# Kernel tuning notes

Hardware: AMD Instinct MI355X
Metric: run time of the kernel (lower is better)

Reference implementation:

```python
import jax, jax.numpy as jnp
import numpy as np

D_MODEL = 2048
N_HEAD = 16
HEAD_DIM = D_MODEL // N_HEAD
D_FF = 8192
SEQ = 2048
PAST = 2048
BATCH = 2
LN_EPS = 1e-5


def setup_inputs() -> dict:
    key = jax.random.key(0)
    ks = jax.random.split(key, 16)
    s = 0.02  # weight init scale
    return {
        "x": jax.random.normal(ks[0], (SEQ, BATCH, D_MODEL), jnp.float32),
        "k_cache": jax.random.normal(ks[1], (PAST, BATCH, N_HEAD, HEAD_DIM), jnp.float32),
        "v_cache": jax.random.normal(ks[2], (PAST, BATCH, N_HEAD, HEAD_DIM), jnp.float32),
        "mask": jnp.zeros((SEQ, PAST + SEQ), jnp.float32),
        "q_w": jax.random.normal(ks[3], (D_MODEL, D_MODEL), jnp.float32) * s,
        "q_b": jnp.zeros((D_MODEL,), jnp.float32),
        "k_w": jax.random.normal(ks[4], (D_MODEL, D_MODEL), jnp.float32) * s,
        "k_b": jnp.zeros((D_MODEL,), jnp.float32),
        "v_w": jax.random.normal(ks[5], (D_MODEL, D_MODEL), jnp.float32) * s,
        "v_b": jnp.zeros((D_MODEL,), jnp.float32),
        "o_w": jax.random.normal(ks[6], (D_MODEL, D_MODEL), jnp.float32) * s,
        "o_b": jnp.zeros((D_MODEL,), jnp.float32),
        "ln1_g": jnp.ones((D_MODEL,), jnp.float32),
        "ln1_b": jnp.zeros((D_MODEL,), jnp.float32),
        "ln2_g": jnp.ones((D_MODEL,), jnp.float32),
        "ln2_b": jnp.zeros((D_MODEL,), jnp.float32),
        "w1": jax.random.normal(ks[7], (D_MODEL, D_FF), jnp.float32) * s,
        "b1": jnp.zeros((D_FF,), jnp.float32),
        "w2": jax.random.normal(ks[8], (D_FF, D_MODEL), jnp.float32) * s,
        "b2": jnp.zeros((D_MODEL,), jnp.float32),
    }


def _layernorm(y, g, b):
    m = jnp.mean(y, axis=-1, keepdims=True)
    v = jnp.var(y, axis=-1, keepdims=True)  # biased var, matches torch LayerNorm
    return (y - m) * jax.lax.rsqrt(v + LN_EPS) * g + b


def reference(x, k_cache, v_cache, mask, q_w, q_b, k_w, k_b, v_w, v_b, o_w, o_b,
              ln1_g, ln1_b, ln2_g, ln2_b, w1, b1, w2, b2):
    S, B, D = x.shape
    H, hd = N_HEAD, HEAD_DIM

    x_norm = _layernorm(x, ln1_g, ln1_b)
    q = (x_norm @ q_w + q_b).reshape(S, B, H, hd)
    k = (x_norm @ k_w + k_b).reshape(S, B, H, hd)
    v = (x_norm @ v_w + v_b).reshape(S, B, H, hd)

    k_full = jnp.concatenate([k_cache, k], axis=0)  # [T,B,H,hd], T = past+S
    v_full = jnp.concatenate([v_cache, v], axis=0)

    # scores: [B,H,S,T]
    scores = jnp.einsum('sbhd,tbhd->bhst', q, k_full) / (hd ** 0.5)
    scores = scores + mask  # mask [S,T] broadcasts over B,H
    attn = jax.nn.softmax(scores, axis=-1)
    out = jnp.einsum('bhst,tbhd->sbhd', attn, v_full).reshape(S, B, D)
    x = x + out @ o_w + o_b

    h = _layernorm(x, ln2_g, ln2_b)
    x = x + jax.nn.gelu(h @ w1 + b1, approximate=False) @ w2 + b2
    return (x, k_full, v_full)
```

## Files before the change

kernel.cpp:

```cpp
#include <hip/hip_runtime.h>
#include <hip/hip_bf16.h>


typedef __bf16 bf16x8 __attribute__((ext_vector_type(8)));
typedef float f32x4 __attribute__((ext_vector_type(4)));
typedef float f32x16 __attribute__((ext_vector_type(16)));
typedef unsigned int u32;

__device__ __forceinline__ unsigned short f2bf(float f) {
  union { float f; unsigned u; } v; v.f = f;
  return (unsigned short)((v.u + 0x7FFFu + ((v.u >> 16) & 1u)) >> 16);
}

__device__ __forceinline__ float fexp2(float x) {
#if __has_builtin(__builtin_amdgcn_exp2f)
  return __builtin_amdgcn_exp2f(x);
#else
  float r;
  asm volatile("v_exp_f32 %0, %1\ns_nop 0" : "=v"(r) : "v"(x));
  return r;
#endif
}

__device__ __forceinline__ float fast_gelu(float x) {
  const float u = 0.7978845608028654f * fmaf(0.044715f * x * x, x, x);
  const float e = fexp2(fminf(u * 2.885390081777927f, 126.f));
  float rcp;
  asm("v_rcp_f32 %0, %1" : "=v"(rcp) : "v"(e + 1.f));
  return x * e * rcp;
}

__device__ __forceinline__ void gl16(const void* g, void* l) {
  __builtin_amdgcn_global_load_lds((__attribute__((address_space(1))) void*)g,
                                   (__attribute__((address_space(3))) void*)l,
                                   16, 0, 0);
}

__global__ __launch_bounds__(256) void wconvT(const float* __restrict__ W,
                                              unsigned short* __restrict__ Wt,
                                              int K, int N) {
  __shared__ float tl[32][33];
  const int k0 = blockIdx.x * 32, n0 = blockIdx.y * 32;
  const int x = threadIdx.x & 31, y = threadIdx.x >> 5;
  for (int i = 0; i < 4; ++i)
    tl[y + i * 8][x] = W[(size_t)(k0 + y + i * 8) * N + n0 + x];
  __syncthreads();
  for (int i = 0; i < 4; ++i)
    Wt[(size_t)(n0 + y + i * 8) * K + k0 + x] = f2bf(tl[x][y + i * 8]);
}

__global__ __launch_bounds__(256) void prep_k(
    const float* __restrict__ x, const float* __restrict__ ln1g,
    const float* __restrict__ ln1b, unsigned short* __restrict__ xn,
    const float* __restrict__ kc, unsigned short* __restrict__ kf,
    float* __restrict__ out_k,
    const float* __restrict__ vc, unsigned short* __restrict__ vft,
    float* __restrict__ out_v,
    const float* __restrict__ mask, u32* __restrict__ mflags,
    const float* __restrict__ q_w, const float* __restrict__ k_w,
    const float* __restrict__ v_w, const float* __restrict__ o_w,
    unsigned short* __restrict__ Wt) {
  __shared__ float tl[32][33];
  __shared__ float red[8];
  const int blk = blockIdx.x;
  const int tid = threadIdx.x;

  if (blk < 4096) {
    const int row = blk;
    const float4* xr = (const float4*)(x + (size_t)row * 2048);
    const float4 xa = xr[tid], xb = xr[tid + 256];
    float s = xa.x + xa.y + xa.z + xa.w + xb.x + xb.y + xb.z + xb.w;
    float q = xa.x * xa.x + xa.y * xa.y + xa.z * xa.z + xa.w * xa.w +
              xb.x * xb.x + xb.y * xb.y + xb.z * xb.z + xb.w * xb.w;
    for (int off = 32; off; off >>= 1) {
      s += __shfl_xor(s, off);
      q += __shfl_xor(q, off);
    }
    const int wv = tid >> 6, ln = tid & 63;
    if (ln == 0) { red[wv] = s; red[4 + wv] = q; }
    __syncthreads();
    s = red[0] + red[1] + red[2] + red[3];
    q = red[4] + red[5] + red[6] + red[7];
    const float mean = s * (1.f / 2048.f);
    const float rstd = rsqrtf(q * (1.f / 2048.f) - mean * mean + 1e-5f);
    const float4 g0 = ((const float4*)ln1g)[tid], g1 = ((const float4*)ln1g)[tid + 256];
    const float4 b0 = ((const float4*)ln1b)[tid], b1 = ((const float4*)ln1b)[tid + 256];
    ushort4 o0, o1;
    o0.x = f2bf((xa.x - mean) * rstd * g0.x + b0.x);
    o0.y = f2bf((xa.y - mean) * rstd * g0.y + b0.y);
    o0.z = f2bf((xa.z - mean) * rstd * g0.z + b0.z);
    o0.w = f2bf((xa.w - mean) * rstd * g0.w + b0.w);
    o1.x = f2bf((xb.x - mean) * rstd * g1.x + b1.x);
    o1.y = f2bf((xb.y - mean) * rstd * g1.y + b1.y);
    o1.z = f2bf((xb.z - mean) * rstd * g1.z + b1.z);
    o1.w = f2bf((xb.w - mean) * rstd * g1.w + b1.w);
    ((ushort4*)(xn + (size_t)row * 2048))[tid] = o0;
    ((ushort4*)(xn + (size_t)row * 2048))[tid + 256] = o1;
  } else if (blk < 12288) {
    const size_t e = ((size_t)(blk - 4096) * 256 + tid) * 4;
    const int r = (int)(e >> 11), c = (int)(e & 2047);
    const int t = r >> 1, b = r & 1, h = c >> 7, d = c & 127;
    const float4 v = *(const float4*)(kc + e);
    ushort4 o;
    o.x = f2bf(v.x); o.y = f2bf(v.y); o.z = f2bf(v.z); o.w = f2bf(v.w);
    *(ushort4*)(kf + ((size_t)((b * 16 + h) * 4096 + t)) * 128 + d) = o;
    *(float4*)(out_k + (size_t)r * 2048 + c) = v;
  } else if (blk < 20480) {
    const int i = blk - 12288;
    const int t0 = (i & 63) * 32, d0 = ((i >> 6) & 3) * 32, bh = i >> 8;
    const int b = bh >> 4, h = bh & 15;
    const int xx = tid & 31, yy = tid >> 5;
    for (int ii = 0; ii < 4; ++ii) {
      const int t = t0 + yy + ii * 8, d = d0 + xx;
      const float v = vc[((size_t)(t * 2 + b) * 16 + h) * 128 + d];
      tl[yy + ii * 8][xx] = v;
      out_v[((size_t)(t * 2 + b) * 16 + h) * 128 + d] = v;
    }
    __syncthreads();
    for (int ii = 0; ii < 4; ++ii) {
      const int d = d0 + yy + ii * 8, t = t0 + xx;
      vft[((size_t)bh * 128 + d) * 4096 + t] = f2bf(tl[xx][yy + ii * 8]);
    }
  } else if (blk < 20736) {
    const int mb = blk - 20480;
    const float4* p = (const float4*)mask + (size_t)mb * 8192 + tid;
    int nz = 0;
#pragma unroll
    for (int ii = 0; ii < 32; ++ii) {
      const float4 v = p[ii * 256];
      nz |= (v.x != 0.f) | (v.y != 0.f) | (v.z != 0.f) | (v.w != 0.f);
    }
    const int r = __syncthreads_or(nz);
    if (tid == 0) mflags[mb] = (u32)r;
  } else {
    const int i = blk - 20736;
    const int k0 = (i & 63) * 32, n0 = ((i >> 6) & 63) * 32, z = i >> 12;
    const float* W = z == 0 ? q_w : (z == 1 ? k_w : (z == 2 ? v_w : o_w));
    unsigned short* dst = Wt + (size_t)z * 2048 * 2048;
    const int xx = tid & 31, yy = tid >> 5;
    for (int ii = 0; ii < 4; ++ii)
      tl[yy + ii * 8][xx] = W[(size_t)(k0 + yy + ii * 8) * 2048 + n0 + xx];
    __syncthreads();
    for (int ii = 0; ii < 4; ++ii)
      dst[(size_t)(n0 + yy + ii * 8) * 2048 + k0 + xx] = f2bf(tl[xx][yy + ii * 8]);
  }
}

__global__ __launch_bounds__(256) void prep2_k(
    const float* __restrict__ x1, const float* __restrict__ ln2g,
    const float* __restrict__ ln2b, unsigned short* __restrict__ hn,
    const float* __restrict__ w1, unsigned short* __restrict__ w1t,
    const float* __restrict__ w2, unsigned short* __restrict__ w2t) {
  __shared__ float tl[32][33];
  __shared__ float red[8];
  const int blk = blockIdx.x;
  const int tid = threadIdx.x;

  if (blk < 4096) {
    const int row = blk;
    const float4* xr = (const float4*)(x1 + (size_t)row * 2048);
    const float4 xa = xr[tid], xb = xr[tid + 256];
    float s = xa.x + xa.y + xa.z + xa.w + xb.x + xb.y + xb.z + xb.w;
    float q = xa.x * xa.x + xa.y * xa.y + xa.z * xa.z + xa.w * xa.w +
              xb.x * xb.x + xb.y * xb.y + xb.z * xb.z + xb.w * xb.w;
    for (int off = 32; off; off >>= 1) {
      s += __shfl_xor(s, off);
      q += __shfl_xor(q, off);
    }
    const int wv = tid >> 6, ln = tid & 63;
    if (ln == 0) { red[wv] = s; red[4 + wv] = q; }
    __syncthreads();
    s = red[0] + red[1] + red[2] + red[3];
    q = red[4] + red[5] + red[6] + red[7];
    const float mean = s * (1.f / 2048.f);
    const float rstd = rsqrtf(q * (1.f / 2048.f) - mean * mean + 1e-5f);
    const float4 g0 = ((const float4*)ln2g)[tid], g1 = ((const float4*)ln2g)[tid + 256];
    const float4 b0 = ((const float4*)ln2b)[tid], b1 = ((const float4*)ln2b)[tid + 256];
    ushort4 o0, o1;
    o0.x = f2bf((xa.x - mean) * rstd * g0.x + b0.x);
    o0.y = f2bf((xa.y - mean) * rstd * g0.y + b0.y);
    o0.z = f2bf((xa.z - mean) * rstd * g0.z + b0.z);
    o0.w = f2bf((xa.w - mean) * rstd * g0.w + b0.w);
    o1.x = f2bf((xb.x - mean) * rstd * g1.x + b1.x);
    o1.y = f2bf((xb.y - mean) * rstd * g1.y + b1.y);
    o1.z = f2bf((xb.z - mean) * rstd * g1.z + b1.z);
    o1.w = f2bf((xb.w - mean) * rstd * g1.w + b1.w);
    ((ushort4*)(hn + (size_t)row * 2048))[tid] = o0;
    ((ushort4*)(hn + (size_t)row * 2048))[tid + 256] = o1;
  } else if (blk < 20480) {
    const int i = blk - 4096;
    const int k0 = (i & 63) * 32, n0 = (i >> 6) * 32;
    const int xx = tid & 31, yy = tid >> 5;
    for (int ii = 0; ii < 4; ++ii)
      tl[yy + ii * 8][xx] = w1[(size_t)(k0 + yy + ii * 8) * 8192 + n0 + xx];
    __syncthreads();
    for (int ii = 0; ii < 4; ++ii)
      w1t[(size_t)(n0 + yy + ii * 8) * 2048 + k0 + xx] = f2bf(tl[xx][yy + ii * 8]);
  } else {
    const int i = blk - 20480;
    const int k0 = (i & 255) * 32, n0 = (i >> 8) * 32;
    const int xx = tid & 31, yy = tid >> 5;
    for (int ii = 0; ii < 4; ++ii)
      tl[yy + ii * 8][xx] = w2[(size_t)(k0 + yy + ii * 8) * 2048 + n0 + xx];
    __syncthreads();
    for (int ii = 0; ii < 4; ++ii)
      w2t[(size_t)(n0 + yy + ii * 8) * 8192 + k0 + xx] = f2bf(tl[xx][yy + ii * 8]);
  }
}

template <int TAG, int EPI>
__global__ __launch_bounds__(512, 2) void gemm8p(
    const unsigned short* __restrict__ A, const unsigned short* __restrict__ Bt,
    const float* __restrict__ bias, const float* __restrict__ bias2,
    const float* __restrict__ bias3,
    float* __restrict__ Cf, unsigned short* __restrict__ Cb,
    float* __restrict__ of2, unsigned short* __restrict__ pb2,
    unsigned short* __restrict__ pb3, int N, int K) {
  __shared__ unsigned short sA[2][256 * 64];
  __shared__ unsigned short sB[2][256 * 64];
  const int tid = threadIdx.x;
  const int wv = tid >> 6, ln = tid & 63;
  const int wm = wv >> 2, wn = wv & 3;
  const int nwg = gridDim.x;
  const int bid = blockIdx.x;
  const int wk = (bid & 7) * (nwg >> 3) + (bid >> 3);
  const int nmt = 16;
  const int m0 = (wk & (nmt - 1)) * 256, n0 = (wk / nmt) * 256;
  const int NT = K >> 6, NI = NT >> 1;

  f32x4 acc[8][4] = {};
  bf16x8 af[4][2], bfr[2][2];

  auto ST = [&](int t, int which, int bb) {
    if (t >= NT) return;
    const unsigned short* G = (which < 2) ? A : Bt;
    const int base0 = ((which < 2) ? m0 : n0) + (which & 1) * 128;
    char* dst = (char*)((which < 2) ? &sA[bb][0] : &sB[bb][0]) + (which & 1) * 16384;
    const size_t kb = (size_t)t * 64;
#pragma unroll
    for (int c = 0; c < 2; ++c) {
      const int o = tid * 16 + c * 8192;
      const int row = o >> 7;
      const int cb = (o & 127) ^ ((row & 7) << 4);
      gl16((const char*)G + ((size_t)(base0 + row) * K + kb) * 2 + cb, dst + o);
    }
  };
  auto LDA = [&](int bb, int mh) {
    const char* base = (const char*)&sA[bb][0];
#pragma unroll
    for (int i = 0; i < 4; ++i) {
      const int r = wm * 128 + mh * 64 + i * 16 + (ln & 15);
#pragma unroll
      for (int kk = 0; kk < 2; ++kk) {
        int aa = (r << 7) + ((ln >> 4) << 4) + kk * 64;
        aa ^= (r & 7) << 4;
        af[i][kk] = *(const bf16x8*)(base + aa);
      }
    }
  };
  auto LDB = [&](int bb, int nh) {
    const char* base = (const char*)&sB[bb][0];
#pragma unroll
    for (int j = 0; j < 2; ++j) {
      const int r = wn * 64 + nh * 32 + j * 16 + (ln & 15);
#pragma unroll
      for (int kk = 0; kk < 2; ++kk) {
        int aa = (r << 7) + ((ln >> 4) << 4) + kk * 64;
        aa ^= (r & 7) << 4;
        bfr[j][kk] = *(const bf16x8*)(base + aa);
      }
    }
  };
  auto MM = [&](int mh, int nh) {
    __builtin_amdgcn_s_setprio(1);
#pragma unroll
    for (int i = 0; i < 4; ++i)
#pragma unroll
      for (int j = 0; j < 2; ++j)
#pragma unroll
        for (int kk = 0; kk < 2; ++kk)
          acc[mh * 4 + i][nh * 2 + j] = __builtin_amdgcn_mfma_f32_16x16x32_bf16(
              af[i][kk], bfr[j][kk], acc[mh * 4 + i][nh * 2 + j], 0, 0, 0);
    __builtin_amdgcn_s_setprio(0);
  };
#define BAR() __builtin_amdgcn_s_barrier()
#define VM2() asm volatile("s_waitcnt vmcnt(2)" ::: "memory")
#define VM0() asm volatile("s_waitcnt vmcnt(0)" ::: "memory")

  ST(0, 0, 0); ST(0, 1, 0); ST(0, 2, 0); ST(0, 3, 0); ST(1, 0, 1);
  VM2();
  BAR();

#pragma unroll 1
  for (int it = 0; it < NI; ++it) {
    const int t1 = 2 * it + 1, t2 = 2 * it + 2, t3 = 2 * it + 3;
    const bool lastit = (it == NI - 1);
    LDA(0, 0); LDB(0, 0); ST(t1, 1, 1); BAR(); MM(0, 0); BAR();
    LDB(0, 1);            ST(t1, 2, 1); BAR(); MM(0, 1); BAR();
    LDA(0, 1);            ST(t1, 3, 1); BAR(); MM(1, 1); BAR();
    LDB(0, 0);            ST(t2, 0, 0); BAR(); MM(1, 0);
    if (lastit) VM0(); else VM2();
    BAR();
    LDA(1, 0); LDB(1, 0); ST(t2, 1, 0); BAR(); MM(0, 0); BAR();
    LDB(1, 1);            ST(t2, 2, 0); BAR(); MM(0, 1); BAR();
    LDA(1, 1);            ST(t2, 3, 0); BAR(); MM(1, 1); BAR();
    LDB(1, 0);            ST(t3, 0, 1); BAR(); MM(1, 0);
    if (!lastit) VM2();
    BAR();
  }
#undef BAR
#undef VM2
#undef VM0

  const int lr = (ln >> 4) << 2, lc = ln & 15;
  if (EPI == 0) {
    const int seg = n0 >> 11;
    const float* bp = seg == 0 ? bias : (seg == 1 ? bias2 : bias3);
#pragma unroll
    for (int f = 0; f < 8; ++f) {
#pragma unroll
      for (int j = 0; j < 4; ++j) {
        const int nn = (n0 & 2047) + wn * 64 + j * 16 + lc;
        const int h = nn >> 7, d = nn & 127;
        const float bv = bp[nn];
#pragma unroll
        for (int r = 0; r < 4; ++r) {
          const int m = m0 + wm * 128 + f * 16 + lr + r;
          const int s = m >> 1, b = m & 1;
          const float v = acc[f][j][r] + bv;
          if (seg == 0) {
            Cb[((size_t)(b * 16 + h) * 2048 + s) * 128 + d] = f2bf(v);
          } else if (seg == 1) {
            pb2[((size_t)(b * 16 + h) * 4096 + 2048 + s) * 128 + d] = f2bf(v);
            Cf[((size_t)((2048 + s) * 2 + b) * 16 + h) * 128 + d] = v;
          } else {
            pb3[((size_t)(b * 16 + h) * 128 + d) * 4096 + 2048 + s] = f2bf(v);
            of2[((size_t)((2048 + s) * 2 + b) * 16 + h) * 128 + d] = v;
          }
        }
      }
    }
  } else {
    char* wbase = (wv < 4) ? (char*)&sA[0][0] + wv * 16384
                           : (char*)&sB[0][0] + (wv - 4) * 16384;
#pragma unroll
    for (int f = 0; f < 8; ++f) {
#pragma unroll
      for (int j = 0; j < 4; ++j) {
        const int nl = j * 16 + lc;
        const float bv = bias[n0 + wn * 64 + nl];
#pragma unroll
        for (int r = 0; r < 4; ++r) {
          const int ml = f * 16 + lr + r;
          const float v = fast_gelu(acc[f][j][r] + bv);
          *(unsigned short*)(wbase + ml * 128 + ((nl * 2) ^ ((ml & 7) << 4))) =
              f2bf(v);
        }
      }
    }
    __syncthreads();
#pragma unroll
    for (int p = 0; p < 16; ++p) {
      const int row = p * 16 + (tid >> 5);
      const int nn = (tid & 31) * 8;
      const int wvv = (row >> 7) * 4 + (nn >> 6);
      const char* rb = (wvv < 4) ? (const char*)&sA[0][0] + wvv * 16384
                                 : (const char*)&sB[0][0] + (wvv - 4) * 16384;
      const int ml = row & 127, nl = nn & 63;
      const int4 val = *(const int4*)(rb + ml * 128 + ((nl * 2) ^ ((ml & 7) << 4)));
      *(int4*)((char*)Cb + ((size_t)(m0 + row) * N + n0 + nn) * 2) = val;
    }
  }
}

template <int TAG, int EPI>
__global__ __launch_bounds__(512, 2) void gemm8n(
    const unsigned short* __restrict__ A, const unsigned short* __restrict__ Bt,
    const float* __restrict__ bias, const float* __restrict__ Rsd,
    float* __restrict__ Cf, int N, int K) {
  __shared__ unsigned short sA[2][128 * 64];
  __shared__ unsigned short sB[2][256 * 64];
  const int tid = threadIdx.x;
  const int wv = tid >> 6, ln = tid & 63;
  const int wm = wv >> 2, wn = wv & 3;
  const int nwg = gridDim.x;
  const int bid = blockIdx.x;
  const int wk = (bid & 7) * (nwg >> 3) + (bid >> 3);
  const int m0 = (wk & 31) * 128, n0 = (wk >> 5) * 256;
  const int NT = K >> 6;

  f32x4 acc[4][4] = {};
  bf16x8 af[2][2], bfr[2][2];

  auto ST = [&](int t, int which, int bb) {
    if (t >= NT) return;
    const unsigned short* G = (which == 0) ? A : Bt;
    const int base0 = (which == 0) ? m0 : (which == 1 ? n0 : n0 + 128);
    char* dst = (which == 0) ? (char*)&sA[bb][0]
                             : (char*)&sB[bb][0] + (which - 1) * 16384;
    const size_t kb = (size_t)t * 64;
#pragma unroll
    for (int c = 0; c < 2; ++c) {
      const int o = tid * 16 + c * 8192;
      const int row = o >> 7;
      const int cb = (o & 127) ^ ((row & 7) << 4);
      gl16((const char*)G + ((size_t)(base0 + row) * K + kb) * 2 + cb, dst + o);
    }
  };
  auto LDA = [&](int bb, int mh) {
    const char* base = (const char*)&sA[bb][0];
#pragma unroll
    for (int i = 0; i < 2; ++i) {
      const int r = wm * 64 + mh * 32 + i * 16 + (ln & 15);
#pragma unroll
      for (int kk = 0; kk < 2; ++kk) {
        int aa = (r << 7) + ((ln >> 4) << 4) + kk * 64;
        aa ^= (r & 7) << 4;
        af[i][kk] = *(const bf16x8*)(base + aa);
      }
    }
  };
  auto LDB = [&](int bb, int nh) {
    const char* base = (const char*)&sB[bb][0];
#pragma unroll
    for (int j = 0; j < 2; ++j) {
      const int r = wn * 64 + nh * 32 + j * 16 + (ln & 15);
#pragma unroll
      for (int kk = 0; kk < 2; ++kk) {
        int aa = (r << 7) + ((ln >> 4) << 4) + kk * 64;
        aa ^= (r & 7) << 4;
        bfr[j][kk] = *(const bf16x8*)(base + aa);
      }
    }
  };
  auto MM = [&](int mh, int nh) {
    __builtin_amdgcn_s_setprio(1);
#pragma unroll
    for (int i = 0; i < 2; ++i)
#pragma unroll
      for (int j = 0; j < 2; ++j)
#pragma unroll
        for (int kk = 0; kk < 2; ++kk)
          acc[mh * 2 + i][nh * 2 + j] = __builtin_amdgcn_mfma_f32_16x16x32_bf16(
              af[i][kk], bfr[j][kk], acc[mh * 2 + i][nh * 2 + j], 0, 0, 0);
    __builtin_amdgcn_s_setprio(0);
  };
#define BAR() __builtin_amdgcn_s_barrier()
#define VM2() asm volatile("s_waitcnt vmcnt(2)" ::: "memory")
#define VM0() asm volatile("s_waitcnt vmcnt(0)" ::: "memory")

  ST(0, 0, 0); ST(0, 1, 0); ST(0, 2, 0); ST(1, 0, 1);
  VM2();
  BAR();

#pragma unroll 1
  for (int t = 0; t < NT; ++t) {
    const int cur = t & 1;
    LDA(cur, 0); LDB(cur, 0); ST(t + 1, 1, cur ^ 1); BAR(); MM(0, 0); BAR();
    LDB(cur, 1); ST(t + 1, 2, cur ^ 1); BAR(); MM(0, 1); BAR();
    LDA(cur, 1); BAR(); MM(1, 1); BAR();
    LDB(cur, 0); ST(t + 2, 0, cur); BAR(); MM(1, 0);
    if (t >= NT - 2) VM0(); else VM2();
    BAR();
  }
#undef BAR
#undef VM2
#undef VM0

  const int lr = (ln >> 4) << 2, lc = ln & 15;
#pragma unroll
  for (int i = 0; i < 4; ++i) {
#pragma unroll
    for (int j = 0; j < 4; ++j) {
      const int n = n0 + wn * 64 + j * 16 + lc;
      const float bv = bias[n];
#pragma unroll
      for (int r = 0; r < 4; ++r) {
        const int m = m0 + wm * 64 + i * 16 + lr + r;
        const float v = acc[i][j][r] + bv + Rsd[(size_t)m * N + n];
        Cf[(size_t)m * N + n] = v;
      }
    }
  }
}

__global__ __launch_bounds__(256, 2) void attn6(
    const unsigned short* __restrict__ Q,
    const unsigned short* __restrict__ Kf,
    const unsigned short* __restrict__ Vt,
    const float* __restrict__ mask,
    const u32* __restrict__ flags,
    unsigned short* __restrict__ ctx) {
  __shared__ __attribute__((aligned(16))) char smem[65536];
  const int tid = threadIdx.x;
  const int wv = tid >> 6;
  const int ln = tid & 63;
  const int q = ln & 31;
  const int hi = ln >> 5;
  const int sw = (q & 7) << 4;
  const int bh = blockIdx.y;
  const int s0w = blockIdx.x * 128 + wv * 32;

  const int mnz = __syncthreads_or((int)flags[tid]);

  bf16x8 qreg[8];
  {
    const char* qsrc = (const char*)Q +
        ((size_t)bh * 2048 + s0w + q) * 256 + (hi << 4);
#pragma unroll
    for (int kk = 0; kk < 8; ++kk) qreg[kk] = *(const bf16x8*)(qsrc + kk * 32);
  }

  const char* kp[8];
  const char* vp[4];
#pragma unroll
  for (int kk = 0; kk < 8; ++kk)
    kp[kk] = smem + (q << 8) + (((kk << 5) + (hi << 4)) ^ sw);
#pragma unroll
  for (int kk = 0; kk < 4; ++kk)
    vp[kk] = smem + 32768 + (q << 7) + (((kk << 5) + (hi << 4)) ^ sw);

  const char* Kg;
  const char* Vg;
  {
    const int oo = tid * 16;
    const int kr = oo >> 8, kc = oo & 255;
    Kg = (const char*)Kf + (size_t)bh * 4096 * 256 + (size_t)kr * 256 +
         (kc ^ ((kr & 7) << 4));
    const int vr = oo >> 7, vc = oo & 127;
    Vg = (const char*)Vt + (size_t)bh * 128 * 8192 + (size_t)vr * 8192 +
         (vc ^ ((vr & 7) << 4));
  }
  char* kdst = smem + tid * 16;
  char* vdst = smem + 32768 + tid * 16;

#define STG(BUF)                                               \
  do {                                                         \
    _Pragma("unroll") for (int is = 0; is < 4; ++is) {         \
      gl16(Kg + is * 4096, kdst + (BUF) + is * 4096);          \
      gl16(Vg + (size_t)is * 262144, vdst + (BUF) + is * 4096);\
    }                                                          \
    Kg += 16384; Vg += 128;                                    \
  } while (0)
#define BARR() __builtin_amdgcn_s_barrier()
#define VMW8() asm volatile("s_waitcnt vmcnt(8)" ::: "memory")
#define VMW0() asm volatile("s_waitcnt vmcnt(0)" ::: "memory")

  f32x16 acc[4] = {};
  float m = -1e30f, l = 0.f;
  const float KLOG = 0.127517445f;

  auto tile = [&](int BUF, int it) {
    f32x16 sc0, sc1;
    {
      f32x16 za = {}, zb = {}, zc = {}, zd = {};
      __builtin_amdgcn_s_setprio(1);
#pragma unroll
      for (int kk = 0; kk < 4; ++kk) {
        za = __builtin_amdgcn_mfma_f32_32x32x16_bf16(
            *(const bf16x8*)(kp[kk] + BUF), qreg[kk], za, 0, 0, 0);
        zb = __builtin_amdgcn_mfma_f32_32x32x16_bf16(
            *(const bf16x8*)(kp[kk + 4] + BUF), qreg[kk + 4], zb, 0, 0, 0);
        zc = __builtin_amdgcn_mfma_f32_32x32x16_bf16(
            *(const bf16x8*)(kp[kk] + BUF + 8192), qreg[kk], zc, 0, 0, 0);
        zd = __builtin_amdgcn_mfma_f32_32x32x16_bf16(
            *(const bf16x8*)(kp[kk + 4] + BUF + 8192), qreg[kk + 4], zd, 0, 0, 0);
      }
      __builtin_amdgcn_s_setprio(0);
      sc0 = za + zb;
      sc1 = zc + zd;
    }

    if (mnz) {
      const float rs = 11.313708498984761f;
#pragma unroll
      for (int r = 0; r < 16; ++r) {
        const int tt = it * 64 + ((r & 3) + ((r >> 2) << 3) + (hi << 2));
        sc0[r] = fmaf(mask[(size_t)(s0w + q) * 4096 + tt], rs, sc0[r]);
        sc1[r] = fmaf(mask[(size_t)(s0w + q) * 4096 + tt + 32], rs, sc1[r]);
      }
    }

    float pmax = sc0[0];
#pragma unroll
    for (int r = 1; r < 16; ++r) pmax = fmaxf(pmax, sc0[r]);
#pragma unroll
    for (int r = 0; r < 16; ++r) pmax = fmaxf(pmax, sc1[r]);
    pmax = fmaxf(pmax, __shfl_xor(pmax, 32));
    if (__any(pmax > m + 90.5f)) {
      const float mn = fmaxf(m, pmax);
      const float corr = fexp2((m - mn) * KLOG);
      m = mn; l *= corr;
#pragma unroll
      for (int d4 = 0; d4 < 4; ++d4)
#pragma unroll
        for (int e = 0; e < 16; ++e) acc[d4][e] *= corr;
    }
    const float mk = m * KLOG;
    float rsum = 0.f;
#pragma unroll
    for (int r = 0; r < 16; ++r) {
      const float e = fexp2(fmaf(sc0[r], KLOG, -mk));
      sc0[r] = e;
      rsum += e;
    }
#pragma unroll
    for (int r = 0; r < 16; ++r) {
      const float e = fexp2(fmaf(sc1[r], KLOG, -mk));
      sc1[r] = e;
      rsum += e;
    }
    rsum += __shfl_xor(rsum, 32);
    l += rsum;

    bf16x8 pw[4];
#pragma unroll
    for (int kk = 0; kk < 4; ++kk) {
      const int rb = (kk & 1) * 8;
      u32 w0, w1, w2, w3;
      if (kk < 2) {
        asm("v_cvt_pk_bf16_f32 %0, %1, %2" : "=v"(w0) : "v"(sc0[rb + 0]), "v"(sc0[rb + 1]));
        asm("v_cvt_pk_bf16_f32 %0, %1, %2" : "=v"(w1) : "v"(sc0[rb + 2]), "v"(sc0[rb + 3]));
        asm("v_cvt_pk_bf16_f32 %0, %1, %2" : "=v"(w2) : "v"(sc0[rb + 4]), "v"(sc0[rb + 5]));
        asm("v_cvt_pk_bf16_f32 %0, %1, %2" : "=v"(w3) : "v"(sc0[rb + 6]), "v"(sc0[rb + 7]));
      } else {
        asm("v_cvt_pk_bf16_f32 %0, %1, %2" : "=v"(w0) : "v"(sc1[rb + 0]), "v"(sc1[rb + 1]));
        asm("v_cvt_pk_bf16_f32 %0, %1, %2" : "=v"(w1) : "v"(sc1[rb + 2]), "v"(sc1[rb + 3]));
        asm("v_cvt_pk_bf16_f32 %0, %1, %2" : "=v"(w2) : "v"(sc1[rb + 4]), "v"(sc1[rb + 5]));
        asm("v_cvt_pk_bf16_f32 %0, %1, %2" : "=v"(w3) : "v"(sc1[rb + 6]), "v"(sc1[rb + 7]));
      }
      asm("v_permlane32_swap_b32 %0, %1" : "+v"(w0), "+v"(w2));
      asm("v_permlane32_swap_b32 %0, %1" : "+v"(w1), "+v"(w3));
      union { u32 u[4]; bf16x8 b; } pk;
      pk.u[0] = w0; pk.u[1] = w1; pk.u[2] = w2; pk.u[3] = w3;
      pw[kk] = pk.b;
    }

#pragma unroll
    for (int d4 = 0; d4 < 4; ++d4) {
      __builtin_amdgcn_s_setprio(1);
#pragma unroll
      for (int kk = 0; kk < 4; ++kk)
        acc[d4] = __builtin_amdgcn_mfma_f32_32x32x16_bf16(
            *(const bf16x8*)(vp[kk] + BUF + d4 * 4096), pw[kk], acc[d4], 0, 0, 0);
      __builtin_amdgcn_s_setprio(0);
    }
  };

  STG(0);
  STG(16384);
#pragma unroll 1
  for (int it2 = 0; it2 < 31; ++it2) {
    VMW8(); BARR();
    tile(0, 2 * it2);
    BARR();
    STG(0);
    VMW8(); BARR();
    tile(16384, 2 * it2 + 1);
    BARR();
    STG(16384);
  }
  VMW8(); BARR();
  tile(0, 62);
  BARR();
  VMW0(); BARR();
  tile(16384, 63);
#undef STG
#undef BARR
#undef VMW8
#undef VMW0

  const float inv = 1.f / l;
  const int b = bh >> 4, h = bh & 15;
  unsigned short* crow = ctx + ((size_t)(s0w + q) * 2 + b) * 2048 + h * 128;
#pragma unroll
  for (int d4 = 0; d4 < 4; ++d4)
#pragma unroll
    for (int rq = 0; rq < 4; ++rq) {
      ushort4 o;
      o.x = f2bf(acc[d4][rq * 4 + 0] * inv);
      o.y = f2bf(acc[d4][rq * 4 + 1] * inv);
      o.z = f2bf(acc[d4][rq * 4 + 2] * inv);
      o.w = f2bf(acc[d4][rq * 4 + 3] * inv);
      *(ushort4*)(crow + d4 * 32 + rq * 8 + hi * 4) = o;
    }
}

extern "C" void kernel_launch(void* const* d_in, const int* in_sizes, int n_in,
                              void* d_out, int out_size, void* d_ws, size_t ws_size,
                              hipStream_t stream) {
  const float* x    = (const float*)d_in[0];
  const float* kc   = (const float*)d_in[1];
  const float* vc   = (const float*)d_in[2];
  const float* mask = (const float*)d_in[3];
  const float* q_w  = (const float*)d_in[4];
  const float* q_b  = (const float*)d_in[5];
  const float* k_w  = (const float*)d_in[6];
  const float* k_b  = (const float*)d_in[7];
  const float* v_w  = (const float*)d_in[8];
  const float* v_b  = (const float*)d_in[9];
  const float* o_w  = (const float*)d_in[10];
  const float* o_b  = (const float*)d_in[11];
  const float* ln1g = (const float*)d_in[12];
  const float* ln1b = (const float*)d_in[13];
  const float* ln2g = (const float*)d_in[14];
  const float* ln2b = (const float*)d_in[15];
  const float* w1   = (const float*)d_in[16];
  const float* b1   = (const float*)d_in[17];
  const float* w2   = (const float*)d_in[18];
  const float* b2   = (const float*)d_in[19];

  float* out_x = (float*)d_out;
  float* out_k = out_x + (size_t)8388608;
  float* out_v = out_k + (size_t)16777216;

  char* ws = (char*)d_ws;
  unsigned short* kf  = (unsigned short*)(ws);
  unsigned short* vft = (unsigned short*)(ws + 33554432);
  unsigned short* Wt  = (unsigned short*)(ws + 67108864);
  float*          x1  = (float*)(ws + 100663296);
  unsigned short* mid = (unsigned short*)ws;
  u32* mflags = (u32*)(ws + 100663296);

  unsigned short* xn  = (unsigned short*)d_out;
  unsigned short* ctx = xn;
  unsigned short* qb  = (unsigned short*)((char*)d_out + 16777216);
  unsigned short* hn  = qb;

  const bool bigws = ws_size >= (size_t)167772160;
  unsigned short* w2t = bigws ? (unsigned short*)(ws + 134217728) : Wt;

  const dim3 b256(256);

  prep_k<<<37120, b256, 0, stream>>>(x, ln1g, ln1b, xn, kc, kf, out_k,
                                     vc, vft, out_v, mask, mflags,
                                     q_w, k_w, v_w, o_w, Wt);

  gemm8p<0, 0><<<384, dim3(512), 0, stream>>>(
      xn, Wt, q_b, k_b, v_b, out_k, qb, out_v, kf, vft, 6144, 2048);

  attn6<<<dim3(16, 32), b256, 0, stream>>>(qb, kf, vft, mask, mflags, ctx);

  gemm8n<1, 1><<<256, dim3(512), 0, stream>>>(
      ctx, Wt + (size_t)6144 * 2048, o_b, x, x1, 2048, 2048);

  prep2_k<<<bigws ? 36864 : 20480, b256, 0, stream>>>(
      x1, ln2g, ln2b, hn, w1, Wt, w2, w2t);

  gemm8p<2, 2><<<512, dim3(512), 0, stream>>>(
      hn, Wt, b1, nullptr, nullptr, nullptr, mid, nullptr, nullptr, nullptr,
      8192, 2048);

  if (!bigws) wconvT<<<dim3(256, 64), b256, 0, stream>>>(w2, Wt, 8192, 2048);

  gemm8n<3, 1><<<256, dim3(512), 0, stream>>>(
      mid, w2t, b2, x1, out_x, 2048, 8192);
}
```

Before: 842.7 us.

## Split attention over KV length into two halves with a combine kernel

The attention kernel now splits the 4096-key sequence into two halves along a new grid z dimension, so twice as many blocks run. Each block uses half the shared memory with separate K and V staging phases, and launch bounds ask for higher occupancy. Each half writes unnormalized bf16 partial outputs plus its running max and sum, and a new combine kernel merges them into the context buffer. This is meant to fix under-filled compute units from the 512-block grid, at the cost of an extra launch, extra memory traffic, bf16 rounding of the partials, and less prefetch depth.

Measured after the change: 1.240 ms. 47.1% more time.

```diff
diff --git a/kernel.cpp b/kernel.cpp
--- a/kernel.cpp
+++ b/kernel.cpp
@@ -10,6 +10,11 @@
 __device__ __forceinline__ unsigned short f2bf(float f) {
   union { float f; unsigned u; } v; v.f = f;
   return (unsigned short)((v.u + 0x7FFFu + ((v.u >> 16) & 1u)) >> 16);
+}
+
+__device__ __forceinline__ float bf2f(unsigned short u) {
+  union { u32 u; float f; } v; v.u = (u32)u << 16;
+  return v.f;
 }
 
 __device__ __forceinline__ float fexp2(float x) {
@@ -484,14 +489,16 @@
   }
 }
 
-__global__ __launch_bounds__(256, 2) void attn6(
+__global__ __launch_bounds__(256, 4) void attn7(
     const unsigned short* __restrict__ Q,
     const unsigned short* __restrict__ Kf,
     const unsigned short* __restrict__ Vt,
     const float* __restrict__ mask,
     const u32* __restrict__ flags,
-    unsigned short* __restrict__ ctx) {
-  __shared__ __attribute__((aligned(16))) char smem[65536];
+    unsigned short* __restrict__ pO0,
+    unsigned short* __restrict__ pO1,
+    float* __restrict__ pml) {
+  __shared__ __attribute__((aligned(16))) char smem[32768];
   const int tid = threadIdx.x;
   const int wv = tid >> 6;
   const int ln = tid & 63;
@@ -499,6 +506,7 @@
   const int hi = ln >> 5;
   const int sw = (q & 7) << 4;
   const int bh = blockIdx.y;
+  const int th = blockIdx.z;
   const int s0w = blockIdx.x * 128 + wv * 32;
 
   const int mnz = __syncthreads_or((int)flags[tid]);
@@ -518,39 +526,47 @@
     kp[kk] = smem + (q << 8) + (((kk << 5) + (hi << 4)) ^ sw);
 #pragma unroll
   for (int kk = 0; kk < 4; ++kk)
-    vp[kk] = smem + 32768 + (q << 7) + (((kk << 5) + (hi << 4)) ^ sw);
+    vp[kk] = smem + 16384 + (q << 7) + (((kk << 5) + (hi << 4)) ^ sw);
 
   const char* Kg;
   const char* Vg;
   {
     const int oo = tid * 16;
     const int kr = oo >> 8, kc = oo & 255;
-    Kg = (const char*)Kf + (size_t)bh * 4096 * 256 + (size_t)kr * 256 +
-         (kc ^ ((kr & 7) << 4));
+    Kg = (const char*)Kf + (size_t)bh * 4096 * 256 + (size_t)th * 2048 * 256 +
+         (size_t)kr * 256 + (kc ^ ((kr & 7) << 4));
     const int vr = oo >> 7, vc = oo & 127;
     Vg = (const char*)Vt + (size_t)bh * 128 * 8192 + (size_t)vr * 8192 +
-         (vc ^ ((vr & 7) << 4));
+         (size_t)th * 4096 + (vc ^ ((vr & 7) << 4));
   }
   char* kdst = smem + tid * 16;
-  char* vdst = smem + 32768 + tid * 16;
-
-#define STG(BUF)                                               \
-  do {                                                         \
-    _Pragma("unroll") for (int is = 0; is < 4; ++is) {         \
-      gl16(Kg + is * 4096, kdst + (BUF) + is * 4096);          \
-      gl16(Vg + (size_t)is * 262144, vdst + (BUF) + is * 4096);\
-    }                                                          \
-    Kg += 16384; Vg += 128;                                    \
+  char* vdst = smem + 16384 + tid * 16;
+
+#define STGK()                                                  \
+  do {                                                          \
+    _Pragma("unroll") for (int is = 0; is < 4; ++is)            \
+        gl16(Kg + is * 4096, kdst + is * 4096);                 \
+    Kg += 16384;                                                \
+  } while (0)
+#define STGV()                                                  \
+  do {                                                          \
+    _Pragma("unroll") for (int is = 0; is < 4; ++is)            \
+        gl16(Vg + (size_t)is * 262144, vdst + is * 4096);       \
+    Vg += 128;                                                  \
   } while (0)
 #define BARR() __builtin_amdgcn_s_barrier()
-#define VMW8() asm volatile("s_waitcnt vmcnt(8)" ::: "memory")
+#define VMW4() asm volatile("s_waitcnt vmcnt(4)" ::: "memory")
 #define VMW0() asm volatile("s_waitcnt vmcnt(0)" ::: "memory")
 
   f32x16 acc[4] = {};
   float m = -1e30f, l = 0.f;
   const float KLOG = 0.127517445f;
 
-  auto tile = [&](int BUF, int it) {
+  STGK(); STGV();
+#pragma unroll 1
+  for (int it = 0; it < 32; ++it) {
+    VMW4();
+    BARR();
     f32x16 sc0, sc1;
     {
       f32x16 za = {}, zb = {}, zc = {}, zd = {};
@@ -558,24 +574,26 @@
 #pragma unroll
       for (int kk = 0; kk < 4; ++kk) {
         za = __builtin_amdgcn_mfma_f32_32x32x16_bf16(
-            *(const bf16x8*)(kp[kk] + BUF), qreg[kk], za, 0, 0, 0);
+            *(const bf16x8*)(kp[kk]), qreg[kk], za, 0, 0, 0);
         zb = __builtin_amdgcn_mfma_f32_32x32x16_bf16(
-            *(const bf16x8*)(kp[kk + 4] + BUF), qreg[kk + 4], zb, 0, 0, 0);
+            *(const bf16x8*)(kp[kk + 4]), qreg[kk + 4], zb, 0, 0, 0);
         zc = __builtin_amdgcn_mfma_f32_32x32x16_bf16(
-            *(const bf16x8*)(kp[kk] + BUF + 8192), qreg[kk], zc, 0, 0, 0);
+            *(const bf16x8*)(kp[kk] + 8192), qreg[kk], zc, 0, 0, 0);
         zd = __builtin_amdgcn_mfma_f32_32x32x16_bf16(
-            *(const bf16x8*)(kp[kk + 4] + BUF + 8192), qreg[kk + 4], zd, 0, 0, 0);
+            *(const bf16x8*)(kp[kk + 4] + 8192), qreg[kk + 4], zd, 0, 0, 0);
       }
       __builtin_amdgcn_s_setprio(0);
       sc0 = za + zb;
       sc1 = zc + zd;
     }
+    BARR();
+    if (it < 31) STGK();
 
     if (mnz) {
       const float rs = 11.313708498984761f;
 #pragma unroll
       for (int r = 0; r < 16; ++r) {
-        const int tt = it * 64 + ((r & 3) + ((r >> 2) << 3) + (hi << 2));
+        const int tt = th * 2048 + it * 64 + ((r & 3) + ((r >> 2) << 3) + (hi << 2));
         sc0[r] = fmaf(mask[(size_t)(s0w + q) * 4096 + tt], rs, sc0[r]);
         sc1[r] = fmaf(mask[(size_t)(s0w + q) * 4096 + tt + 32], rs, sc1[r]);
       }
@@ -636,54 +654,70 @@
       pw[kk] = pk.b;
     }
 
+    if (it < 31) VMW4(); else VMW0();
+    BARR();
 #pragma unroll
     for (int d4 = 0; d4 < 4; ++d4) {
       __builtin_amdgcn_s_setprio(1);
 #pragma unroll
       for (int kk = 0; kk < 4; ++kk)
         acc[d4] = __builtin_amdgcn_mfma_f32_32x32x16_bf16(
-            *(const bf16x8*)(vp[kk] + BUF + d4 * 4096), pw[kk], acc[d4], 0, 0, 0);
+            *(const bf16x8*)(vp[kk] + d4 * 4096), pw[kk], acc[d4], 0, 0, 0);
       __builtin_amdgcn_s_setprio(0);
     }
-  };
-
-  STG(0);
-  STG(16384);
-#pragma unroll 1
-  for (int it2 = 0; it2 < 31; ++it2) {
-    VMW8(); BARR();
-    tile(0, 2 * it2);
     BARR();
-    STG(0);
-    VMW8(); BARR();
-    tile(16384, 2 * it2 + 1);
-    BARR();
-    STG(16384);
-  }
-  VMW8(); BARR();
-  tile(0, 62);
-  BARR();
-  VMW0(); BARR();
-  tile(16384, 63);
-#undef STG
+    if (it < 31) STGV();
+  }
+#undef STGK
+#undef STGV
 #undef BARR
-#undef VMW8
+#undef VMW4
 #undef VMW0
 
-  const float inv = 1.f / l;
-  const int b = bh >> 4, h = bh & 15;
-  unsigned short* crow = ctx + ((size_t)(s0w + q) * 2 + b) * 2048 + h * 128;
+  const int rg = bh * 2048 + s0w + q;
+  unsigned short* pO = (th == 0) ? pO0 : pO1;
+  unsigned short* orow = pO + (size_t)rg * 128;
 #pragma unroll
   for (int d4 = 0; d4 < 4; ++d4)
 #pragma unroll
     for (int rq = 0; rq < 4; ++rq) {
       ushort4 o;
-      o.x = f2bf(acc[d4][rq * 4 + 0] * inv);
-      o.y = f2bf(acc[d4][rq * 4 + 1] * inv);
-      o.z = f2bf(acc[d4][rq * 4 + 2] * inv);
-      o.w = f2bf(acc[d4][rq * 4 + 3] * inv);
-      *(ushort4*)(crow + d4 * 32 + rq * 8 + hi * 4) = o;
-    }
+      o.x = f2bf(acc[d4][rq * 4 + 0]);
+      o.y = f2bf(acc[d4][rq * 4 + 1]);
+      o.z = f2bf(acc[d4][rq * 4 + 2]);
+      o.w = f2bf(acc[d4][rq * 4 + 3]);
+      *(ushort4*)(orow + d4 * 32 + rq * 8 + hi * 4) = o;
+    }
+  if (hi == 0) {
+    pml[(size_t)(th * 2 + 0) * 65536 + rg] = m;
+    pml[(size_t)(th * 2 + 1) * 65536 + rg] = l;
+  }
+}
+
+__global__ __launch_bounds__(256) void cmb_k(
+    const unsigned short* __restrict__ pO0,
+    const unsigned short* __restrict__ pO1,
+    const float* __restrict__ pml,
+    unsigned short* __restrict__ ctx) {
+  const int e4 = (blockIdx.x * 256 + threadIdx.x) * 4;
+  const int rg = e4 >> 7, d = e4 & 127;
+  const int bh = rg >> 11, row = rg & 2047;
+  const float m0 = pml[rg], l0 = pml[65536 + rg];
+  const float m1 = pml[131072 + rg], l1 = pml[196608 + rg];
+  const float KLOG = 0.127517445f;
+  const float mm = fmaxf(m0, m1);
+  const float s0 = fexp2((m0 - mm) * KLOG);
+  const float s1 = fexp2((m1 - mm) * KLOG);
+  const float inv = 1.f / (l0 * s0 + l1 * s1);
+  const ushort4 a = *(const ushort4*)(pO0 + (size_t)rg * 128 + d);
+  const ushort4 c = *(const ushort4*)(pO1 + (size_t)rg * 128 + d);
+  ushort4 o;
+  o.x = f2bf((bf2f(a.x) * s0 + bf2f(c.x) * s1) * inv);
+  o.y = f2bf((bf2f(a.y) * s0 + bf2f(c.y) * s1) * inv);
+  o.z = f2bf((bf2f(a.z) * s0 + bf2f(c.z) * s1) * inv);
+  o.w = f2bf((bf2f(a.w) * s0 + bf2f(c.w) * s1) * inv);
+  const int b = bh >> 4, h = bh & 15;
+  *(ushort4*)(ctx + (size_t)(row * 2 + b) * 2048 + h * 128 + d) = o;
 }
 
 extern "C" void kernel_launch(void* const* d_in, const int* in_sizes, int n_in,
@@ -720,11 +754,14 @@
   unsigned short* Wt  = (unsigned short*)(ws + 67108864);
   float*          x1  = (float*)(ws + 100663296);
   unsigned short* mid = (unsigned short*)ws;
-  u32* mflags = (u32*)(ws + 100663296);
+  u32*   mflags = (u32*)(ws + 100663296);
+  float* pml    = (float*)(ws + 100663296 + 4096);
+  unsigned short* pO1 = (unsigned short*)(ws + 100663296 + 2097152);
 
   unsigned short* xn  = (unsigned short*)d_out;
-  unsigned short* ctx = xn;
+  unsigned short* pO0 = xn;
   unsigned short* qb  = (unsigned short*)((char*)d_out + 16777216);
+  unsigned short* ctx = qb;
   unsigned short* hn  = qb;
 
   const bool bigws = ws_size >= (size_t)167772160;
@@ -739,7 +776,9 @@
   gemm8p<0, 0><<<384, dim3(512), 0, stream>>>(
       xn, Wt, q_b, k_b, v_b, out_k, qb, out_v, kf, vft, 6144, 2048);
 
-  attn6<<<dim3(16, 32), b256, 0, stream>>>(qb, kf, vft, mask, mflags, ctx);
+  attn7<<<dim3(16, 32, 2), b256, 0, stream>>>(qb, kf, vft, mask, mflags,
+                                              pO0, pO1, pml);
+  cmb_k<<<8192, b256, 0, stream>>>(pO0, pO1, pml, ctx);
 
   gemm8n<1, 1><<<256, dim3(512), 0, stream>>>(
       ctx, Wt + (size_t)6144 * 2048, o_b, x, x1, 2048, 2048);
```
